# Optimization experiments

Hardware: AMD Instinct MI355X
Metric: run time of the kernel (lower is better)

The kernel has to match this reference:

```python
import jax, jax.numpy as jnp
import numpy as np

NUM_CLASSES = 21
POS_THR = 0.5
ALPHA = 0.5
GAMMA = 1.5
EPS = 1e-6


def _rand_boxes(key, prefix):
    k1, k2 = jax.random.split(key)
    xy = jax.random.uniform(k1, prefix + (2,)) * 0.8
    wh = jax.random.uniform(k2, prefix + (2,)) * 0.18 + 0.02
    return jnp.concatenate([xy, xy + wh], axis=-1)


def setup_inputs() -> dict:
    key = jax.random.key(0)
    B, A, T, C = 16, 65536, 64, NUM_CLASSES
    ks = jax.random.split(key, 6)
    anchors = _rand_boxes(ks[0], (A,))
    bbox_pred = _rand_boxes(ks[1], (B, A))
    target_boxes = _rand_boxes(ks[2], (B, T))
    conf_pred = jax.random.uniform(ks[3], (B, A))          # probabilities in [0,1)
    cls_pred = jax.random.normal(ks[4], (B, A, C - 1))     # logits
    target_labels = jax.random.randint(ks[5], (B, T), 1, C)  # labels in 1..C-1
    return {
        "bbox_pred": bbox_pred,
        "conf_pred": conf_pred,
        "cls_pred": cls_pred,
        "anchors": anchors,
        "target_boxes": target_boxes,
        "target_labels": target_labels,
    }


def _pairwise_iou(b1, b2):
    # b1: [A,4], b2: [T,4] -> [A,T]
    x1 = jnp.maximum(b1[:, None, 0], b2[None, :, 0])
    y1 = jnp.maximum(b1[:, None, 1], b2[None, :, 1])
    x2 = jnp.minimum(b1[:, None, 2], b2[None, :, 2])
    y2 = jnp.minimum(b1[:, None, 3], b2[None, :, 3])
    inter = jnp.clip(x2 - x1, 0) * jnp.clip(y2 - y1, 0)
    a1 = (b1[:, 2] - b1[:, 0]) * (b1[:, 3] - b1[:, 1])
    a2 = (b2[:, 2] - b2[:, 0]) * (b2[:, 3] - b2[:, 1])
    union = a1[:, None] + a2[None, :] - inter
    return inter / (union + EPS)


def _giou_loss(b1, b2):
    # elementwise over matched pairs, b1/b2: [A,4] -> [A]
    x1 = jnp.maximum(b1[:, 0], b2[:, 0]); y1 = jnp.maximum(b1[:, 1], b2[:, 1])
    x2 = jnp.minimum(b1[:, 2], b2[:, 2]); y2 = jnp.minimum(b1[:, 3], b2[:, 3])
    inter = jnp.clip(x2 - x1, 0) * jnp.clip(y2 - y1, 0)
    a1 = (b1[:, 2] - b1[:, 0]) * (b1[:, 3] - b1[:, 1])
    a2 = (b2[:, 2] - b2[:, 0]) * (b2[:, 3] - b2[:, 1])
    union = a1 + a2 - inter
    iou = inter / (union + EPS)
    ex1 = jnp.minimum(b1[:, 0], b2[:, 0]); ey1 = jnp.minimum(b1[:, 1], b2[:, 1])
    ex2 = jnp.maximum(b1[:, 2], b2[:, 2]); ey2 = jnp.maximum(b1[:, 3], b2[:, 3])
    enc = (ex2 - ex1) * (ey2 - ey1)
    giou = iou - (enc - union) / (enc + EPS)
    return 1.0 - giou


def _per_image(bbox_p, conf_p, cls_p, anchors, t_boxes, t_labels):
    ious = _pairwise_iou(anchors, t_boxes)            # [A,T]
    max_ious = ious.max(axis=1)                       # [A]
    best_target_idx = jnp.argmax(ious, axis=1)        # [A]
    best_anchor_idx = jnp.argmax(ious, axis=0)        # [T]
    pos = (max_ious >= POS_THR).at[best_anchor_idx].set(True)
    ct = pos.astype(conf_p.dtype)                     # conf target
    alpha_factor = jnp.where(pos, 1.0 - ALPHA, ALPHA)
    focal_w = ((1.0 - conf_p) * ct + conf_p * (1.0 - ct)) ** GAMMA
    bce = -(ct * jnp.log(conf_p + EPS) + (1.0 - ct) * jnp.log(1.0 - conf_p + EPS))
    conf_loss = (bce * focal_w * alpha_factor).mean()

    matched_boxes = t_boxes[best_target_idx]          # [A,4]
    giou_l = _giou_loss(bbox_p, matched_boxes)        # [A]
    l1_l = jnp.abs(bbox_p - matched_boxes).mean(axis=1)
    npos = jnp.maximum(ct.sum(), 1.0)
    bbox_loss = (((giou_l + 0.5 * l1_l) * ct).sum()) / npos

    matched_labels = t_labels[best_target_idx]        # [A]
    onehot = jax.nn.one_hot(matched_labels - 1, NUM_CLASSES - 1, dtype=cls_p.dtype)
    # stable BCE with logits, mean over classes per anchor
    x = cls_p
    bce_cls = jnp.maximum(x, 0) - x * onehot + jnp.log1p(jnp.exp(-jnp.abs(x)))
    cls_loss = ((bce_cls.mean(axis=1)) * ct).sum() / npos
    return conf_loss, bbox_loss, cls_loss


def reference(bbox_pred, conf_pred, cls_pred, anchors, target_boxes, target_labels):
    conf_l, bbox_l, cls_l = jax.vmap(
        _per_image, in_axes=(0, 0, 0, None, 0, 0)
    )(bbox_pred, conf_pred, cls_pred, anchors, target_boxes, target_labels)
    conf_loss = conf_l.mean(); bbox_loss = bbox_l.mean(); cls_loss = cls_l.mean()
    total = conf_loss + bbox_loss + cls_loss  # weights all 1.0 (defaults)
    return total, conf_loss, bbox_loss, cls_loss
```

## Files before the change

### kernel.cpp

```cpp
#include <hip/hip_runtime.h>
#include <stdint.h>
#include <math.h>

#define A_N 65536
#define B_N 16
#define T_N 64
#define NB  (A_N / 256)
#define EPSF 1e-6f
#define LN2F   0.69314718055994531f
#define LOG2EF 1.4426950408889634f

#define EXP2F(x) __builtin_amdgcn_exp2f(x)
#define LOG2F(x) __builtin_amdgcn_logf(x)
#define RCPF(x)  __builtin_amdgcn_rcpf(x)
#define SQRTF(x) __builtin_amdgcn_sqrtf(x)


__device__ __forceinline__ float iou_fast(float4 an, float a1, float4 t4, float tar)
{
    float x1 = fmaxf(an.x, t4.x), y1 = fmaxf(an.y, t4.y);
    float x2 = fminf(an.z, t4.z), y2 = fminf(an.w, t4.w);
    float inter = fmaxf(x2 - x1, 0.f) * fmaxf(y2 - y1, 0.f);
    float ue = ((a1 + tar) - inter) + EPSF;
    return inter * RCPF(ue);
}

__device__ __forceinline__ float conf_term(float p, bool pos)
{
    float u = pos ? p : (1.f - p);
    float w = 1.f - u;
    float bce = -LN2F * LOG2F(u + EPSF);
    float fw = w * SQRTF(w);
    return bce * fw * 0.5f;
}

__device__ __forceinline__ float softplus_negabs(float x)
{
    float y = EXP2F(fabsf(x) * -LOG2EF);
    return LN2F * LOG2F(1.0f + y);
}

__device__ __forceinline__ float cls_term(const float4* cp, const float* cls_f,
                                          size_t ba, int lab)
{
    float s2 = 0.f;
    #pragma unroll
    for (int q = 0; q < 5; ++q) {
        float4 v = cp[q];
        s2 += fmaxf(v.x, 0.f) + softplus_negabs(v.x);
        s2 += fmaxf(v.y, 0.f) + softplus_negabs(v.y);
        s2 += fmaxf(v.z, 0.f) + softplus_negabs(v.z);
        s2 += fmaxf(v.w, 0.f) + softplus_negabs(v.w);
    }
    float xl = cls_f[ba * 20 + (size_t)lab];
    return (s2 - xl) * (1.f / 20.f);
}

__device__ __forceinline__ float bterm_at(float4 pb, float4 mb)
{
    float x1 = fmaxf(pb.x, mb.x), y1 = fmaxf(pb.y, mb.y);
    float x2 = fminf(pb.z, mb.z), y2 = fminf(pb.w, mb.w);
    float inter = fmaxf(x2 - x1, 0.f) * fmaxf(y2 - y1, 0.f);
    float pa1 = (pb.z - pb.x) * (pb.w - pb.y);
    float pa2 = (mb.z - mb.x) * (mb.w - mb.y);
    float uni = pa1 + pa2 - inter;
    float iou = inter * RCPF(uni + EPSF);
    float ex1 = fminf(pb.x, mb.x), ey1 = fminf(pb.y, mb.y);
    float ex2 = fmaxf(pb.z, mb.z), ey2 = fmaxf(pb.w, mb.w);
    float enc = (ex2 - ex1) * (ey2 - ey1);
    float giou = iou - (enc - uni) * RCPF(enc + EPSF);
    float l1 = 0.25f * (fabsf(pb.x - mb.x) + fabsf(pb.y - mb.y) +
                        fabsf(pb.z - mb.z) + fabsf(pb.w - mb.w));
    return (1.f - giou) + 0.5f * l1;
}

__device__ __forceinline__ void resolve_p1(
    unsigned int w, int base, float4 an, float a1,
    const float4* tb, const float* ta, unsigned int* slot_hi,
    unsigned int& bb, int& bt, unsigned int& m2)
{
    m2 = 0u;
    while (w) {
        int z = __builtin_clz(w);
        unsigned int bit = 0x80000000u >> z;
        w &= ~bit;
        int s = base + z;
        float iou = iou_fast(an, a1, tb[s], ta[s]);
        unsigned int u = __float_as_uint(iou);
        if (u > bb) { bb = u; bt = s; }
        unsigned int old = atomicMax(&slot_hi[s], u);
        if (u >= old) m2 |= bit;
    }
}

__device__ __forceinline__ void resolve_p2(
    unsigned int m2, int base, float4 an, float a1,
    const float4* tb, const float* ta, const unsigned int* slot_hi,
    unsigned int* slot_lo, unsigned int lo)
{
    while (m2) {
        int z = __builtin_clz(m2);
        m2 &= ~(0x80000000u >> z);
        int s = base + z;
        float iou = iou_fast(an, a1, tb[s], ta[s]);
        if (__float_as_uint(iou) == slot_hi[s]) atomicMax(&slot_lo[s], lo);
    }
}

__global__ __launch_bounds__(256) void k1_main(
    const float4* __restrict__ anchors,
    const float4* __restrict__ bbox,
    const float*  __restrict__ conf,
    const float4* __restrict__ cls,
    const float4* __restrict__ tboxes,
    const int*    __restrict__ tlabels,
    unsigned long long* __restrict__ keys,
    unsigned char* __restrict__ code,
    float4* __restrict__ partials,
    unsigned int* __restrict__ done)
{
    __shared__ float4 tb[T_N];
    __shared__ float  ta[T_N];
    __shared__ float  rhsv[T_N];
    __shared__ int    tl[T_N];
    __shared__ unsigned int slot_hi[T_N];
    __shared__ unsigned int slot_lo[T_N];
    const int b   = blockIdx.y;
    const int tid = threadIdx.x;
    if (tid < T_N) {
        float4 t = tboxes[b * T_N + tid];
        float ar = (t.z - t.x) * (t.w - t.y);
        tb[tid] = t;
        ta[tid] = ar;
        rhsv[tid] = 0.2493f * (ar + EPSF);
        tl[tid] = tlabels[b * T_N + tid];
        slot_hi[tid] = 0u;
        slot_lo[tid] = 0u;
    }
    if (tid == 0 && blockIdx.x == 0 && b == 0) *done = 0u;
    __syncthreads();

    const int a = blockIdx.x * 256 + tid;
    const float4 an = anchors[a];
    const float a1 = (an.z - an.x) * (an.w - an.y);
    const float npa = -0.2493f * a1;
    const unsigned int lo = ~(unsigned int)a;

    unsigned int mlo = 0u, mhi = 0u;
    #pragma unroll 8
    for (int s = 0; s < 32; ++s) {
        float4 t4 = tb[s];
        float r  = rhsv[s];
        float x1 = fmaxf(an.x, t4.x), y1 = fmaxf(an.y, t4.y);
        float x2 = fminf(an.z, t4.z), y2 = fminf(an.w, t4.w);
        float inter = fmaxf(x2 - x1, 0.f) * fmaxf(y2 - y1, 0.f);
        mlo = mlo + mlo + ((fmaf(1.2493f, inter, npa) >= r) ? 1u : 0u);
    }
    #pragma unroll 8
    for (int s = 32; s < 64; ++s) {
        float4 t4 = tb[s];
        float r  = rhsv[s];
        float x1 = fmaxf(an.x, t4.x), y1 = fmaxf(an.y, t4.y);
        float x2 = fminf(an.z, t4.z), y2 = fminf(an.w, t4.w);
        float inter = fmaxf(x2 - x1, 0.f) * fmaxf(y2 - y1, 0.f);
        mhi = mhi + mhi + ((fmaf(1.2493f, inter, npa) >= r) ? 1u : 0u);
    }

    unsigned int bb = 0u; int bt = 0;
    unsigned int m2lo, m2hi;
    resolve_p1(mlo,  0, an, a1, tb, ta, slot_hi, bb, bt, m2lo);
    resolve_p1(mhi, 32, an, a1, tb, ta, slot_hi, bb, bt, m2hi);
    __syncthreads();
    resolve_p2(m2lo,  0, an, a1, tb, ta, slot_hi, slot_lo, lo);
    resolve_p2(m2hi, 32, an, a1, tb, ta, slot_hi, slot_lo, lo);

    const bool thr = (bb >= 0x3F000000u);
    const size_t ba = (size_t)b * A_N + a;
    code[ba] = (unsigned char)(bt | (thr ? 128 : 0));

    float r0 = conf_term(conf[ba], thr);
    float r2 = 0.f, r3 = 0.f;
    if (thr) {
        r2 = bterm_at(bbox[ba], tb[bt]);
        r3 = cls_term(cls + ba * 5, (const float*)cls, ba, tl[bt] - 1);
    }
    const float r1 = (float)__popcll(__ballot(thr));

    #pragma unroll
    for (int off = 32; off; off >>= 1) {
        r0 += __shfl_down(r0, off, 64);
        r2 += __shfl_down(r2, off, 64);
        r3 += __shfl_down(r3, off, 64);
    }
    __shared__ float4 red[4];
    const int wv = tid >> 6;
    if ((tid & 63) == 0) red[wv] = make_float4(r0, r1, r2, r3);
    __syncthreads();
    if (tid == 0) {
        float4 v;
        v.x = red[0].x + red[1].x + red[2].x + red[3].x;
        v.y = red[0].y + red[1].y + red[2].y + red[3].y;
        v.z = red[0].z + red[1].z + red[2].z + red[3].z;
        v.w = red[0].w + red[1].w + red[2].w + red[3].w;
        partials[(size_t)b * NB + blockIdx.x] = v;
    }
    if (tid < T_N)
        keys[(((size_t)b * NB + blockIdx.x) << 6) | tid] =
            ((unsigned long long)slot_hi[tid] << 32) | (unsigned long long)slot_lo[tid];
}

__global__ __launch_bounds__(1024) void k2_all(
    const unsigned long long* __restrict__ keys,
    const float4* __restrict__ anchors,
    const float4* __restrict__ bbox,
    const float*  __restrict__ conf,
    const float4* __restrict__ cls,
    const float4* __restrict__ tboxes,
    const int*    __restrict__ tlabels,
    const unsigned char* __restrict__ code,
    const float4* __restrict__ partials,
    float* __restrict__ lossImg,
    unsigned int* __restrict__ done,
    float* __restrict__ out)
{
    __shared__ unsigned long long sh[16][64];
    __shared__ unsigned long long sw[16];
    __shared__ float4 tb[T_N];
    __shared__ float  ta[T_N];
    __shared__ unsigned int winner[64];
    __shared__ int emptyList[64];
    __shared__ int nEmpty;
    __shared__ float4 corr;
    __shared__ float4 redf[4];
    __shared__ int lastFlag;
    const int b = blockIdx.x, tid = threadIdx.x;
    const int t = tid & 63, g = tid >> 6;
    if (tid == 0) nEmpty = 0;
    if (tid < T_N) {
        float4 tt = tboxes[b * T_N + tid];
        tb[tid] = tt;
        ta[tid] = (tt.z - tt.x) * (tt.w - tt.y);
    }

    unsigned long long K = 0ull;
    #pragma unroll 4
    for (int i = 0; i < 16; ++i) {
        unsigned long long k = keys[(((size_t)b * NB + (g * 16 + i)) << 6) | t];
        if (k > K) K = k;
    }
    sh[g][t] = K;
    __syncthreads();
    if (tid < 64) {
        unsigned long long m = sh[0][tid];
        #pragma unroll
        for (int g2 = 1; g2 < 16; ++g2) if (sh[g2][tid] > m) m = sh[g2][tid];
        unsigned int lo32 = (unsigned int)(m & 0xFFFFFFFFull);
        if (lo32 != 0u) winner[tid] = ~lo32;
        else { int i = atomicAdd(&nEmpty, 1); emptyList[i] = tid; }
    }
    __syncthreads();

    const int ne = nEmpty;
    for (int e = 0; e < ne; ++e) {
        const int tt = emptyList[e];
        const float4 tbx = tb[tt];
        const float tar = ta[tt];
        unsigned long long bk = 0ull;
        for (int i = tid; i < A_N; i += 1024) {
            float4 an = anchors[i];
            float a1 = (an.z - an.x) * (an.w - an.y);
            float iou = iou_fast(an, a1, tbx, tar);
            unsigned long long key = ((unsigned long long)__float_as_uint(iou) << 32)
                                   | (unsigned long long)(~(unsigned int)i);
            if (key > bk) bk = key;
        }
        #pragma unroll
        for (int off = 32; off; off >>= 1) {
            unsigned long long o = __shfl_down(bk, off, 64);
            if (o > bk) bk = o;
        }
        if ((tid & 63) == 0) sw[g] = bk;
        __syncthreads();
        if (tid == 0) {
            unsigned long long m = sw[0];
            #pragma unroll
            for (int i = 1; i < 16; ++i) if (sw[i] > m) m = sw[i];
            winner[tt] = ~(unsigned int)(m & 0xFFFFFFFFull);
        }
        __syncthreads();
    }

    if (tid < 64) {
        const unsigned int wa = winner[tid];
        bool owner = true;
        for (int k = 0; k < 64; ++k) {
            unsigned int o = __shfl(wa, k, 64);
            if (k < tid && o == wa) owner = false;
        }
        const size_t ba = (size_t)b * A_N + wa;
        float d0 = 0.f, d1 = 0.f, d2 = 0.f, d3 = 0.f;
        if (owner && (code[ba] & 128) == 0) {
            const float4 aw = anchors[wa];
            const float aw1 = (aw.z - aw.x) * (aw.w - aw.y);
            unsigned int bb = 0u; int bt = 0;
            for (int s = 0; s < T_N; ++s) {
                float iou = iou_fast(aw, aw1, tb[s], ta[s]);
                unsigned int u = __float_as_uint(iou);
                if (u > bb) { bb = u; bt = s; }
            }
            const float p = conf[ba];
            d0 = conf_term(p, true) - conf_term(p, false);
            d1 = 1.f;
            d2 = bterm_at(bbox[ba], tb[bt]);
            d3 = cls_term(cls + ba * 5, (const float*)cls, ba,
                          tlabels[b * T_N + bt] - 1);
        }
        #pragma unroll
        for (int off = 32; off; off >>= 1) {
            d0 += __shfl_down(d0, off, 64);
            d1 += __shfl_down(d1, off, 64);
            d2 += __shfl_down(d2, off, 64);
            d3 += __shfl_down(d3, off, 64);
        }
        if (tid == 0) corr = make_float4(d0, d1, d2, d3);
    }
    __syncthreads();

    if (tid < NB) {
        float4 v = partials[(size_t)b * NB + tid];
        #pragma unroll
        for (int off = 32; off; off >>= 1) {
            v.x += __shfl_down(v.x, off, 64);
            v.y += __shfl_down(v.y, off, 64);
            v.z += __shfl_down(v.z, off, 64);
            v.w += __shfl_down(v.w, off, 64);
        }
        if ((tid & 63) == 0) redf[tid >> 6] = v;
    }
    __syncthreads();
    if (tid == 0) {
        float s0 = redf[0].x + redf[1].x + redf[2].x + redf[3].x + corr.x;
        float s1 = redf[0].y + redf[1].y + redf[2].y + redf[3].y + corr.y;
        float s2 = redf[0].z + redf[1].z + redf[2].z + redf[3].z + corr.z;
        float s3 = redf[0].w + redf[1].w + redf[2].w + redf[3].w + corr.w;
        float npos = fmaxf(s1, 1.f);
        atomicExch(&lossImg[b * 3 + 0], s0 * (1.f / (float)A_N));
        atomicExch(&lossImg[b * 3 + 1], s2 / npos);
        atomicExch(&lossImg[b * 3 + 2], s3 / npos);
        __threadfence();
        unsigned int old = atomicAdd(done, 1u);
        lastFlag = (old == B_N - 1) ? 1 : 0;
    }
    __syncthreads();

    if (lastFlag && tid < 64) {
        __threadfence();
        float c = 0.f, bm = 0.f, l = 0.f;
        if (tid < B_N) {
            c  = atomicAdd(&lossImg[tid * 3 + 0], 0.f);
            bm = atomicAdd(&lossImg[tid * 3 + 1], 0.f);
            l  = atomicAdd(&lossImg[tid * 3 + 2], 0.f);
        }
        #pragma unroll
        for (int off = 8; off; off >>= 1) {
            c  += __shfl_down(c,  off, 64);
            bm += __shfl_down(bm, off, 64);
            l  += __shfl_down(l,  off, 64);
        }
        if (tid == 0) {
            c *= (1.f / 16.f); bm *= (1.f / 16.f); l *= (1.f / 16.f);
            out[0] = c + bm + l;
            out[1] = c;
            out[2] = bm;
            out[3] = l;
        }
    }
}

extern "C" void kernel_launch(void* const* d_in, const int* in_sizes, int n_in,
                              void* d_out, int out_size, void* d_ws, size_t ws_size,
                              hipStream_t stream)
{
    const float4* bbox    = (const float4*)d_in[0];
    const float*  conf    = (const float*) d_in[1];
    const float4* cls     = (const float4*)d_in[2];
    const float4* anchors = (const float4*)d_in[3];
    const float4* tboxes  = (const float4*)d_in[4];
    const int*    tlabels = (const int*)   d_in[5];
    float* out = (float*)d_out;

    char* ws = (char*)d_ws;
    unsigned long long* keys  = (unsigned long long*)ws;
    unsigned char*      code  = (unsigned char*)(ws + (2u << 20));
    float4*       partials = (float4*)(ws + (3u << 20));
    float*        lossImg  = (float*)(ws + (3u << 20) + (64u << 10));
    unsigned int* done     = (unsigned int*)(ws + (3u << 20) + (64u << 10) + 256);

    k1_main <<<dim3(NB, B_N), 256, 0, stream>>>(anchors, bbox, conf, cls, tboxes,
                                                tlabels, keys, code, partials, done);
    k2_all  <<<B_N, 1024, 0, stream>>>(keys, anchors, bbox, conf, cls, tboxes,
                                       tlabels, code, partials, lossImg, done, out);
}
```

Baseline: 57.96 us.

## Replace dense anchor-target prefilter with 8x8 spatial grid cell masks

Builds per-block 8x8 grid cell bitmasks of which targets overlap each cell. Each anchor then ORs the masks of the cells it covers instead of running the 64-target inequality prefilter. The exact prefilter test moves into resolve_p1 and gates the atomicMax, so candidates are checked only for targets that pass the grid test. The cost is an extra shared-memory build phase, a barrier, and data-dependent loops over cells that may diverge across a wavefront.

After: 55.25 us. -4.7%, faster.

```diff
diff --git a/kernel.cpp b/kernel.cpp
--- a/kernel.cpp
+++ b/kernel.cpp
@@ -75,9 +75,9 @@
 }
 
 __device__ __forceinline__ void resolve_p1(
-    unsigned int w, int base, float4 an, float a1,
-    const float4* tb, const float* ta, unsigned int* slot_hi,
-    unsigned int& bb, int& bt, unsigned int& m2)
+    unsigned int w, int base, float4 an, float a1, float npa,
+    const float4* tb, const float* ta, const float* rhsv,
+    unsigned int* slot_hi, unsigned int& bb, int& bt, unsigned int& m2)
 {
     m2 = 0u;
     while (w) {
@@ -85,11 +85,18 @@
         unsigned int bit = 0x80000000u >> z;
         w &= ~bit;
         int s = base + z;
-        float iou = iou_fast(an, a1, tb[s], ta[s]);
+        float4 t4 = tb[s];
+        float x1 = fmaxf(an.x, t4.x), y1 = fmaxf(an.y, t4.y);
+        float x2 = fminf(an.z, t4.z), y2 = fminf(an.w, t4.w);
+        float inter = fmaxf(x2 - x1, 0.f) * fmaxf(y2 - y1, 0.f);
+        float ue = ((a1 + ta[s]) - inter) + EPSF;
+        float iou = inter * RCPF(ue);
         unsigned int u = __float_as_uint(iou);
         if (u > bb) { bb = u; bt = s; }
-        unsigned int old = atomicMax(&slot_hi[s], u);
-        if (u >= old) m2 |= bit;
+        if (fmaf(1.2493f, inter, npa) >= rhsv[s]) {
+            unsigned int old = atomicMax(&slot_hi[s], u);
+            if (u >= old) m2 |= bit;
+        }
     }
 }
 
@@ -125,6 +132,8 @@
     __shared__ int    tl[T_N];
     __shared__ unsigned int slot_hi[T_N];
     __shared__ unsigned int slot_lo[T_N];
+    __shared__ unsigned int cellm_lo[64];
+    __shared__ unsigned int cellm_hi[64];
     const int b   = blockIdx.y;
     const int tid = threadIdx.x;
     if (tid < T_N) {
@@ -136,46 +145,63 @@
         tl[tid] = tlabels[b * T_N + tid];
         slot_hi[tid] = 0u;
         slot_lo[tid] = 0u;
+        cellm_lo[tid] = 0u;
+        cellm_hi[tid] = 0u;
     }
     if (tid == 0 && blockIdx.x == 0 && b == 0) *done = 0u;
     __syncthreads();
 
+    {
+        const int c  = tid & 63;
+        const int pr = tid >> 6;
+        const int cx = c & 7, cy = c >> 3;
+        const float clx = cx * 0.125f, chx = clx + 0.125f;
+        const float cly = cy * 0.125f, chy = cly + 0.125f;
+        unsigned int pm = 0u;
+        const int t0 = pr * 16;
+        #pragma unroll
+        for (int j = 0; j < 16; ++j) {
+            int t = t0 + j;
+            float4 t4 = tb[t];
+            bool hit = (t4.x <= chx) && (t4.z >= clx) &&
+                       (t4.y <= chy) && (t4.w >= cly);
+            pm |= hit ? (0x80000000u >> (t & 31)) : 0u;
+        }
+        if (pr < 2) atomicOr(&cellm_lo[c], pm);
+        else        atomicOr(&cellm_hi[c], pm);
+    }
+    __syncthreads();
+
     const int a = blockIdx.x * 256 + tid;
+    const size_t ba = (size_t)b * A_N + a;
     const float4 an = anchors[a];
     const float a1 = (an.z - an.x) * (an.w - an.y);
     const float npa = -0.2493f * a1;
     const unsigned int lo = ~(unsigned int)a;
 
     unsigned int mlo = 0u, mhi = 0u;
-    #pragma unroll 8
-    for (int s = 0; s < 32; ++s) {
-        float4 t4 = tb[s];
-        float r  = rhsv[s];
-        float x1 = fmaxf(an.x, t4.x), y1 = fmaxf(an.y, t4.y);
-        float x2 = fminf(an.z, t4.z), y2 = fminf(an.w, t4.w);
-        float inter = fmaxf(x2 - x1, 0.f) * fmaxf(y2 - y1, 0.f);
-        mlo = mlo + mlo + ((fmaf(1.2493f, inter, npa) >= r) ? 1u : 0u);
-    }
-    #pragma unroll 8
-    for (int s = 32; s < 64; ++s) {
-        float4 t4 = tb[s];
-        float r  = rhsv[s];
-        float x1 = fmaxf(an.x, t4.x), y1 = fmaxf(an.y, t4.y);
-        float x2 = fminf(an.z, t4.z), y2 = fminf(an.w, t4.w);
-        float inter = fmaxf(x2 - x1, 0.f) * fmaxf(y2 - y1, 0.f);
-        mhi = mhi + mhi + ((fmaf(1.2493f, inter, npa) >= r) ? 1u : 0u);
+    {
+        const int cx0 = min(7, (int)(an.x * 8.f));
+        const int cx1 = min(7, (int)(an.z * 8.f));
+        const int cy0 = min(7, (int)(an.y * 8.f));
+        const int cy1 = min(7, (int)(an.w * 8.f));
+        for (int cy = cy0; cy <= cy1; ++cy)
+            for (int cx = cx0; cx <= cx1; ++cx) {
+                int c = cy * 8 + cx;
+                mlo |= cellm_lo[c];
+                mhi |= cellm_hi[c];
+            }
     }
 
     unsigned int bb = 0u; int bt = 0;
     unsigned int m2lo, m2hi;
-    resolve_p1(mlo,  0, an, a1, tb, ta, slot_hi, bb, bt, m2lo);
-    resolve_p1(mhi, 32, an, a1, tb, ta, slot_hi, bb, bt, m2hi);
+    resolve_p1(mlo,  0, an, a1, npa, tb, ta, rhsv, slot_hi, bb, bt, m2lo);
+    resolve_p1(mhi, 32, an, a1, npa, tb, ta, rhsv, slot_hi, bb, bt, m2hi);
     __syncthreads();
     resolve_p2(m2lo,  0, an, a1, tb, ta, slot_hi, slot_lo, lo);
     resolve_p2(m2hi, 32, an, a1, tb, ta, slot_hi, slot_lo, lo);
 
     const bool thr = (bb >= 0x3F000000u);
-    const size_t ba = (size_t)b * A_N + a;
     code[ba] = (unsigned char)(bt | (thr ? 128 : 0));
 
     float r0 = conf_term(conf[ba], thr);
```
